# Kernel optimization log

Hardware: AMD Instinct MI355X
Metric: run time of the kernel (lower is better)

Reference implementation:

```python
import jax, jax.numpy as jnp
import numpy as np

# ---- straight-through binary quantizers (custom VJP matches torch autograd.Functions) ----
@jax.custom_vjp
def bq(x):
    return jnp.sign(x)
def _bq_fwd(x):
    return jnp.sign(x), x
def _bq_bwd(x, g):
    return (g * ((x > -1.0) & (x < 1.0)).astype(g.dtype),)
bq.defvjp(_bq_fwd, _bq_bwd)

@jax.custom_vjp
def bq_quad(x):
    return jnp.sign(x)
def _bqq_fwd(x):
    return jnp.sign(x), x
def _bqq_bwd(x, g):
    return (jnp.maximum(2.0 - jnp.abs(2.0 * x), 0.0) * g,)
bq_quad.defvjp(_bqq_fwd, _bqq_bwd)

def bilinear(x, W, s, b):
    # BiLinear: row-centered sign weights scaled by learned per-row factor, sign activations
    Wc = W - jnp.mean(W, axis=-1, keepdims=True)
    Wb = s * bq(Wc)                      # (out, in)
    return bq(x) @ Wb.T + b

def selective_scan(u, delta, A, Bs, Cs, D, delta_bias):
    # u, delta: (B,K,Dn,L); A: (K,Dn,N); Bs,Cs: (B,K,N,L); D, delta_bias: (K,Dn)
    Bn, K, Dn, L = u.shape
    N = A.shape[-1]
    delta = jax.nn.softplus(delta + delta_bias[None, :, :, None])
    def step(h, inp):
        ut, dt, Bt, Ct = inp             # (B,K,Dn),(B,K,Dn),(B,K,N),(B,K,N)
        dA = jnp.exp(dt[..., None] * A[None])
        h = dA * h + (dt * ut)[..., None] * Bt[:, :, None, :]
        y = jnp.einsum('bkdn,bkn->bkd', h, Ct)
        return h, y
    h0 = jnp.zeros((Bn, K, Dn, N), u.dtype)
    _, ys = jax.lax.scan(step, h0,
                         (u.transpose(3, 0, 1, 2), delta.transpose(3, 0, 1, 2),
                          Bs.transpose(3, 0, 1, 2), Cs.transpose(3, 0, 1, 2)))
    y = ys.transpose(1, 2, 3, 0)         # (B,K,Dn,L)
    return y + D[None, :, :, None] * u

def _forward(x, W_in, b_in, s_in, move0_b, conv_W, conv_b, rp_b0, prelu_a, rp_b1,
             Wl, bl, sl, Wd, bd, sd, dt_bias, A_logs, Ds, ln_w, ln_b, W_out, b_out, s_out):
    Bn, H, Wi, dm = x.shape
    Dn = conv_W.shape[0]
    K = 4
    N = A_logs.shape[1]
    R = Wd.shape[2]
    L = H * Wi
    xz = bilinear(x, W_in, s_in, b_in)                  # (B,H,W,2*Dn)
    xp, z = jnp.split(xz, 2, axis=-1)
    xc = xp.transpose(0, 3, 1, 2)                       # (B,Dn,H,W)
    # BConv2d: move0 bias -> sign (quad STE) -> binary conv -> RPReLU -> residual
    t = bq_quad(xc + move0_b[None, :, None, None])
    sc = jax.lax.stop_gradient(jnp.mean(jnp.abs(conv_W), axis=(1, 2, 3), keepdims=True))
    cw = jnp.clip(conv_W, -1.0, 1.0)
    Wb = jax.lax.stop_gradient(sc * jnp.sign(conv_W) - cw) + cw
    t = jax.lax.conv_general_dilated(t, Wb, (1, 1), [(1, 1), (1, 1)],
                                     dimension_numbers=('NCHW', 'OIHW', 'NCHW'))
    t = t + conv_b[None, :, None, None]
    t = t + rp_b0[None, :, None, None]
    t = jnp.where(t >= 0, t, prelu_a[None, :, None, None] * t)
    t = t + rp_b1[None, :, None, None] + xc
    xconv = jax.nn.silu(t)
    # 4-direction scan inputs
    x_flat = xconv.reshape(Bn, Dn, L)
    x_tr = xconv.transpose(0, 1, 3, 2).reshape(Bn, Dn, L)
    x_hwwh = jnp.stack([x_flat, x_tr], axis=1)
    xs = jnp.concatenate([x_hwwh, jnp.flip(x_hwwh, axis=-1)], axis=1)   # (B,K,Dn,L)
    # NOTE: torch does .view(B,L,-1) on contiguous (B,Dn,L) slices = raw reshape (not transpose)
    xin = xs.reshape(Bn, K, L, Dn)
    x_dbl = jax.vmap(bilinear, in_axes=(1, 0, 0, 0), out_axes=1)(xin, Wl, sl, bl)  # (B,K,L,R+2N)
    x_dbl = x_dbl.transpose(0, 1, 3, 2)                                 # (B,K,R+2N,L)
    dts_r, Bs, Cs = jnp.split(x_dbl, [R, R + N], axis=2)
    dts_in = dts_r.reshape(Bn, K, L, R)  # raw reshape, matches torch .view
    dts = jax.vmap(bilinear, in_axes=(1, 0, 0, 0), out_axes=1)(dts_in, Wd, sd, bd)  # (B,K,L,Dn)
    dts = dts.transpose(0, 1, 3, 2)                                     # (B,K,Dn,L)
    A = -jnp.exp(A_logs).reshape(K, Dn, N)
    out_y = selective_scan(xs, dts, A, Bs, Cs, Ds.reshape(K, Dn), dt_bias.reshape(K, Dn))
    inv_y = jnp.flip(out_y[:, 2:4], axis=-1)
    wh_y = out_y[:, 1].reshape(Bn, Dn, Wi, H).transpose(0, 1, 3, 2).reshape(Bn, Dn, L)
    invwh_y = inv_y[:, 1].reshape(Bn, Dn, Wi, H).transpose(0, 1, 3, 2).reshape(Bn, Dn, L)
    y = out_y[:, 0] + inv_y[:, 0] + wh_y + invwh_y                      # (B,Dn,L)
    y = y.transpose(0, 2, 1).reshape(Bn, H, Wi, Dn)
    mu = jnp.mean(y, axis=-1, keepdims=True)
    var = jnp.var(y, axis=-1, keepdims=True)
    y = (y - mu) / jnp.sqrt(var + 1e-5) * ln_w + ln_b                   # LayerNorm eps=1e-5
    y = y * jax.nn.silu(z)
    return bilinear(y, W_out, s_out, b_out)

def setup_inputs():
    key = jax.random.key(0)
    ks = jax.random.split(key, 12)
    B, H, Wi, dm = 4, 64, 64, 96
    Dn, N, R, K = 192, 16, 6, 4
    u = lambda k, sh, a: jax.random.uniform(k, sh, jnp.float32, -a, a)
    x = jax.random.normal(ks[0], (B, H, Wi, dm), jnp.float32)
    W_in = u(ks[1], (2 * Dn, dm), 0.015)
    b_in = u(ks[2], (2 * Dn,), 0.01)
    s_in = jnp.mean(jnp.abs(W_in), axis=1, keepdims=True)
    move0_b = jnp.zeros((Dn,), jnp.float32)
    conv_W = 0.05 * jax.random.normal(ks[3], (Dn, Dn, 3, 3), jnp.float32)
    conv_b = u(ks[4], (Dn,), 0.01)
    rp_b0 = jnp.zeros((Dn,), jnp.float32)
    prelu_a = 0.25 * jnp.ones((Dn,), jnp.float32)
    rp_b1 = jnp.zeros((Dn,), jnp.float32)
    Wl = u(ks[5], (K, R + 2 * N, Dn), 0.015)
    bl = u(ks[6], (K, R + 2 * N), 0.01)
    sl = jnp.mean(jnp.abs(Wl), axis=2, keepdims=True)
    std = R ** -0.5
    Wd = u(ks[7], (K, Dn, R), std)
    bd = u(ks[8], (K, Dn), 0.01)
    sd = jnp.mean(jnp.abs(Wd), axis=2, keepdims=True)
    dt = jnp.exp(jax.random.uniform(ks[9], (K * Dn,), jnp.float32)
                 * (np.log(0.1) - np.log(0.001)) + np.log(0.001))
    dt = jnp.clip(dt, 1e-4, None)
    dt_bias = dt + jnp.log(-jnp.expm1(-dt))
    A_logs = jnp.tile(jnp.log(jnp.arange(1, N + 1, dtype=jnp.float32))[None, :], (K * Dn, 1))
    Ds = jnp.ones((K * Dn,), jnp.float32)
    ln_w = jnp.ones((Dn,), jnp.float32)
    ln_b = jnp.zeros((Dn,), jnp.float32)
    W_out = u(ks[10], (dm, Dn), 0.015)
    b_out = u(ks[11], (dm,), 0.01)
    s_out = jnp.mean(jnp.abs(W_out), axis=1, keepdims=True)
    return dict(x=x, W_in=W_in, b_in=b_in, s_in=s_in, move0_b=move0_b, conv_W=conv_W,
                conv_b=conv_b, rp_b0=rp_b0, prelu_a=prelu_a, rp_b1=rp_b1, Wl=Wl, bl=bl,
                sl=sl, Wd=Wd, bd=bd, sd=sd, dt_bias=dt_bias, A_logs=A_logs, Ds=Ds,
                ln_w=ln_w, ln_b=ln_b, W_out=W_out, b_out=b_out, s_out=s_out)

def reference(x, W_in, b_in, s_in, move0_b, conv_W, conv_b, rp_b0, prelu_a, rp_b1,
              Wl, bl, sl, Wd, bd, sd, dt_bias, A_logs, Ds, ln_w, ln_b, W_out, b_out, s_out):
    return _forward(x, W_in, b_in, s_in, move0_b, conv_W, conv_b, rp_b0, prelu_a, rp_b1,
                    Wl, bl, sl, Wd, bd, sd, dt_bias, A_logs, Ds, ln_w, ln_b, W_out, b_out, s_out)
```

## Files before the change

### kernel.cpp

```cpp
#include <hip/hip_runtime.h>
#include <math.h>
#include <stdint.h>

#define BB 4
#define HH 64
#define WW2 64
#define DM 96
#define DN 192
#define KK 4
#define NN 16
#define RR 6
#define LL 4096
#define RN 38

#define LOG2E 1.4426950408889634f
#define LN2   0.6931471805599453f

#define OFF_WDB      0
#define OFF_WCS      4608
#define OFF_WAUX     15360
#define OFF_WSC      16896
#define OFF_WBIB     17088
#define OFF_WOUTB    18240
#define OFF_WLBB     18816
#define OFF_XBP      19728
#define OFF_PXS      19728
#define OFF_SSUM     19728
#define OFF_YB       19728
#define OFF_XC       412992
#define OFF_ZS       3558720
#define OFF_XCONV    6704448
#define OFF_XS       9850176
#define OFF_XDBL     22433088
#define OFF_HEND     OFF_XCONV

#define PLANE 4356

__device__ __forceinline__ float fsign(float v) {
  return (v > 0.f) ? 1.f : ((v < 0.f) ? -1.f : 0.f);
}
__device__ __forceinline__ float softplusf(float v) {
  return fmaxf(v, 0.f) + LN2 * log2f(1.f + exp2f(-fabsf(v) * LOG2E));
}
__device__ __forceinline__ float siluf(float v) {
  return v / (1.f + expf(-v));
}
__device__ __forceinline__ float waveAllSum(float s) {
  #pragma unroll
  for (int off = 32; off; off >>= 1) s += __shfl_xor(s, off, 64);
  return s;
}

__global__ __launch_bounds__(64) void k_prep(
    const float* __restrict__ W_in, const float* __restrict__ s_in,
    const float* __restrict__ W_out, const float* __restrict__ s_out,
    const float* __restrict__ Wl, const float* __restrict__ sl,
    const float* __restrict__ Wd, const float* __restrict__ sd,
    const float* __restrict__ convW, float* __restrict__ ws) {
  int r = blockIdx.x, lane = threadIdx.x;
  if (r < 384) {
    const float* row = W_in + r * DM;
    float s = 0.f;
    for (int c = lane; c < DM; c += 64) s += row[c];
    s = waveAllSum(s);
    float mean = s / (float)DM;
    if (lane < 3) {
      uint32_t wv = 0;
      #pragma unroll
      for (int i = 0; i < 32; ++i) wv |= (row[lane * 32 + i] - mean > 0.f ? 1u : 0u) << i;
      ((uint32_t*)(ws + OFF_WBIB))[r * 3 + lane] = wv;
    }
  } else if (r < 480) {
    int m = r - 384;
    const float* row = W_out + m * DN;
    float s = 0.f;
    for (int c = lane; c < DN; c += 64) s += row[c];
    s = waveAllSum(s);
    float mean = s / (float)DN;
    if (lane < 6) {
      uint32_t wv = 0;
      #pragma unroll
      for (int i = 0; i < 32; ++i) wv |= (row[lane * 32 + i] - mean > 0.f ? 1u : 0u) << i;
      ((uint32_t*)(ws + OFF_WOUTB))[m * 6 + lane] = wv;
    }
  } else if (r < 632) {
    int idx = r - 480;
    const float* row = Wl + idx * DN;
    float s = 0.f;
    for (int c = lane; c < DN; c += 64) s += row[c];
    s = waveAllSum(s);
    float mean = s / (float)DN;
    if (lane < 6) {
      uint32_t wv = 0;
      #pragma unroll
      for (int i = 0; i < 32; ++i) wv |= (row[lane * 32 + i] - mean > 0.f ? 1u : 0u) << i;
      ((uint32_t*)(ws + OFF_WLBB))[idx * 6 + lane] = wv;
    }
  } else if (r < 1400) {
    int idx = r - 632;
    const float* row = Wd + idx * RR;
    float s = (lane < RR) ? row[lane] : 0.f;
    s = waveAllSum(s);
    float mean = s / (float)RR;
    unsigned long long mb = __ballot((lane < RR) && (row[lane] - mean > 0.f));
    if (lane == 0) {
      ((uint32_t*)(ws + OFF_WDB))[idx] = (uint32_t)mb & 0x3Fu;
      (ws + OFF_WDB)[768 + idx] = sd[idx];
    }
  } else {
    int o = r - 1400;
    const float* row = convW + o * 1728;
    float s = 0.f;
    for (int j = lane; j < 1728; j += 64) s += fabsf(row[j]);
    s = waveAllSum(s);
    float sc = s / 1728.f;
    uint32_t* wb = (uint32_t*)(ws + OFF_WCS);
    int* aux = (int*)(ws + OFF_WAUX);
    float* scf = ws + OFF_WSC;
    uint32_t word = 0;
    if (lane < 54) {
      int cw = lane / 9, tap = lane % 9;
      #pragma unroll
      for (int i = 0; i < 32; ++i)
        word |= (row[(cw * 32 + i) * 9 + tap] > 0.f ? 1u : 0u) << i;
      wb[o * 56 + lane] = word;
    } else if (lane < 56) {
      wb[o * 56 + lane] = 0u;
    }
    int pc = (lane < 54) ? 2 * (int)__popc(word) - 32 : 0;
    int tapid = lane % 9;
    int wst = 0;
    #pragma unroll
    for (int cw = 0; cw < 6; ++cw) wst += __shfl(pc, cw * 9 + tapid, 64);
    int w_t[9];
    #pragma unroll
    for (int t9 = 0; t9 < 9; ++t9) w_t[t9] = __shfl(wst, t9, 64);
    if (lane == 0) {
      aux[o * 8 + 0] = w_t[0] + w_t[3] + w_t[6];
      aux[o * 8 + 1] = w_t[2] + w_t[5] + w_t[8];
      aux[o * 8 + 2] = w_t[0] + w_t[1] + w_t[2];
      aux[o * 8 + 3] = w_t[6] + w_t[7] + w_t[8];
      aux[o * 8 + 4] = w_t[0];
      aux[o * 8 + 5] = w_t[2];
      aux[o * 8 + 6] = w_t[6];
      aux[o * 8 + 7] = w_t[8];
      scf[o] = sc;
    }
  }
}

__global__ __launch_bounds__(384) void k_bilin_in(
    const float* __restrict__ x, const float* __restrict__ b_in,
    const float* __restrict__ s_in, const float* __restrict__ ws,
    float* __restrict__ xc, float* __restrict__ zs) {
  __shared__ uint32_t spx[16 * 3];
  __shared__ float sxz[384 * 17];
  int p0 = blockIdx.x * 16;
  if (threadIdx.x < 48) {
    int pix = threadIdx.x / 3, wd = threadIdx.x % 3;
    const float* base = x + (size_t)(p0 + pix) * DM + wd * 32;
    uint32_t wv = 0;
    #pragma unroll
    for (int i = 0; i < 32; ++i) wv |= (base[i] > 0.f ? 1u : 0u) << i;
    spx[pix * 3 + wd] = wv;
  }
  __syncthreads();
  int o = threadIdx.x;
  uint32_t w0, w1, w2;
  {
    const uint32_t* wb = (const uint32_t*)(ws + OFF_WBIB) + o * 3;
    w0 = wb[0]; w1 = wb[1]; w2 = wb[2];
  }
  float bias = b_in[o], sc = s_in[o];
  #pragma unroll
  for (int pix = 0; pix < 16; ++pix) {
    int P = (int)__popc(spx[pix * 3 + 0] ^ w0) + (int)__popc(spx[pix * 3 + 1] ^ w1) +
            (int)__popc(spx[pix * 3 + 2] ^ w2);
    sxz[o * 17 + pix] = bias + sc * (float)(DM - 2 * P);
  }
  __syncthreads();
  int b = p0 >> 12, l0 = p0 & 4095;
  for (int f = threadIdx.x; f < DN * 16; f += 384) {
    int od = f >> 4, pix = f & 15;
    xc[((size_t)(b * DN + od)) * LL + l0 + pix] = sxz[od * 17 + pix];
  }
  for (int f = threadIdx.x; f < DN * 16; f += 384) {
    int pix = f / DN, oz = f - pix * DN;
    zs[(size_t)(p0 + pix) * DN + oz] = siluf(sxz[(DN + oz) * 17 + pix]);
  }
}

__global__ __launch_bounds__(256) void k_pack(
    const float* __restrict__ xc, const float* __restrict__ move0,
    uint32_t* __restrict__ xb) {
  int t = blockIdx.x * 256 + threadIdx.x;
  int w2 = t & 31;
  int h = (t >> 5) & 63;
  int g = t >> 11;
  int cw = g % 6, b = g / 6;
  const float* xp = xc + ((size_t)(b * DN + cw * 32)) * LL + h * 64 + w2 * 2;
  uint32_t w0 = 0, w1 = 0;
  #pragma unroll
  for (int i = 0; i < 32; ++i) {
    float m = move0[cw * 32 + i];
    float2 v = *(const float2*)(xp + (size_t)i * LL);
    w0 |= (v.x + m > 0.f ? 1u : 0u) << i;
    w1 |= (v.y + m > 0.f ? 1u : 0u) << i;
  }
  uint32_t* plane = xb + (size_t)(b * 6 + cw) * PLANE;
  plane[(h + 1) * 66 + 1 + w2 * 2] = w0;
  plane[(h + 1) * 66 + 2 + w2 * 2] = w1;
}

__global__ __launch_bounds__(256) void k_conv(
    const uint32_t* __restrict__ xb, const float* __restrict__ xc,
    const uint32_t* __restrict__ wbits, const int* __restrict__ aux,
    const float* __restrict__ scf, const float* __restrict__ conv_b,
    const float* __restrict__ rp_b0, const float* __restrict__ prelu_a,
    const float* __restrict__ rp_b1, float* __restrict__ xconv) {
  int og = blockIdx.x & 3;
  int stripe = (blockIdx.x >> 2) & 15;
  int b = blockIdx.x >> 6;
  int w = threadIdx.x & 63, r = threadIdx.x >> 6;
  int h = stripe * 4 + r;

  __shared__ uint32_t swb[48 * 56];
  __shared__ int saux[48 * 8];
  __shared__ float sconst[48 * 4];
  for (int i = threadIdx.x; i < 48 * 56; i += 256) swb[i] = wbits[og * (48 * 56) + i];
  for (int i = threadIdx.x; i < 48 * 8; i += 256) saux[i] = aux[og * (48 * 8) + i];
  if (threadIdx.x < 48) {
    int o = og * 48 + threadIdx.x;
    sconst[threadIdx.x * 4 + 0] = scf[o];
    sconst[threadIdx.x * 4 + 1] = conv_b[o] + rp_b0[o];
    sconst[threadIdx.x * 4 + 2] = prelu_a[o];
    sconst[threadIdx.x * 4 + 3] = rp_b1[o];
  }

  uint32_t xw[6][9];
  const uint32_t* xpb = xb + (size_t)b * 6 * PLANE;
  #pragma unroll
  for (int cw = 0; cw < 6; ++cw) {
    const uint32_t* plane = xpb + cw * PLANE + (h + 1) * 66 + (w + 1);
    #pragma unroll
    for (int dy = 0; dy < 3; ++dy) {
      #pragma unroll
      for (int dx = 0; dx < 3; ++dx)
        xw[cw][dy * 3 + dx] = plane[(dy - 1) * 66 + (dx - 1)];
    }
  }
  bool isL = (w == 0), isR = (w == 63);
  bool isT = (h == 0), isB = (h == 63);
  const float* xcp = xc + ((size_t)(b * DN + og * 48)) * LL + h * 64 + w;
  float* xop = xconv + ((size_t)(b * DN + og * 48)) * LL + h * 64 + w;
  __syncthreads();

  #pragma unroll 1
  for (int oc = 0; oc < 48; ++oc) {
    const uint32_t* wp = &swb[oc * 56];
    int P = 0;
    #pragma unroll
    for (int cw = 0; cw < 6; ++cw) {
      int pp = 0;
      #pragma unroll
      for (int t = 0; t < 9; ++t) pp += (int)__popc(wp[cw * 9 + t] ^ xw[cw][t]);
      P += pp;
    }
    int corr = isL ? saux[oc * 8 + 0] : (isR ? saux[oc * 8 + 1] : 0);
    if (isT) {
      corr += saux[oc * 8 + 2];
      if (isL) corr -= saux[oc * 8 + 4];
      if (isR) corr -= saux[oc * 8 + 5];
    }
    if (isB) {
      corr += saux[oc * 8 + 3];
      if (isL) corr -= saux[oc * 8 + 6];
      if (isR) corr -= saux[oc * 8 + 7];
    }
    float acc = sconst[oc * 4 + 0] * (float)(1728 - 2 * P + corr);
    float t = acc + sconst[oc * 4 + 1];
    t = (t >= 0.f) ? t : sconst[oc * 4 + 2] * t;
    t += sconst[oc * 4 + 3] + *xcp;
    *xop = siluf(t);
    xcp += LL; xop += LL;
  }
}

__global__ __launch_bounds__(256) void k_build_xs(const float* __restrict__ xconv,
                                                  float* __restrict__ xs,
                                                  uint32_t* __restrict__ pxs) {
  __shared__ float tile[64][65];
  int bd = blockIdx.x;
  int b = bd / DN, d = bd % DN;
  const float* img = xconv + (size_t)bd * LL;
  for (int i = threadIdx.x; i < LL; i += 256)
    tile[i >> 6][i & 63] = img[i];
  __syncthreads();
  int lane = threadIdx.x & 63;
  #pragma unroll
  for (int k = 0; k < 4; ++k) {
    size_t base = ((size_t)((b * KK + k) * DN + d)) * LL;
    for (int j = threadIdx.x; j < LL; j += 256) {
      float v;
      if (k == 0)      v = tile[j >> 6][j & 63];
      else if (k == 1) v = tile[j & 63][j >> 6];
      else if (k == 2) { int t2 = 4095 - j; v = tile[t2 >> 6][t2 & 63]; }
      else             { int t2 = 4095 - j; v = tile[t2 & 63][t2 >> 6]; }
      xs[base + j] = v;
      unsigned long long m = __ballot(v > 0.f);
      if (lane == 0)       pxs[(base + j) >> 5] = (uint32_t)m;
      else if (lane == 32) pxs[(base + j) >> 5] = (uint32_t)(m >> 32);
    }
  }
}

__global__ __launch_bounds__(256) void k_xdbl(
    const uint32_t* __restrict__ pxs, const float* __restrict__ ws,
    const float* __restrict__ bl, const float* __restrict__ sl,
    float* __restrict__ xdbl) {
  int bk = blockIdx.x >> 4;
  int l = ((blockIdx.x & 15) << 8) + threadIdx.x;
  int k = bk & 3;
  __shared__ uint32_t swl[RN * 6];
  __shared__ float sbias[RN], ssc[RN];
  if (threadIdx.x < RN * 6) swl[threadIdx.x] = ((const uint32_t*)(ws + OFF_WLBB))[k * RN * 6 + threadIdx.x];
  if (threadIdx.x < RN) {
    sbias[threadIdx.x] = bl[k * RN + threadIdx.x];
    ssc[threadIdx.x] = sl[k * RN + threadIdx.x];
  }
  uint32_t xb[6];
  const uint32_t* pp = pxs + (size_t)bk * 24576 + (size_t)l * 6;
  #pragma unroll
  for (int j = 0; j < 6; ++j) xb[j] = pp[j];
  __syncthreads();
  float* xo = xdbl + (size_t)bk * (RN * LL) + l;
  #pragma unroll 1
  for (int o = 0; o < RN; ++o) {
    int P = 0;
    #pragma unroll
    for (int j = 0; j < 6; ++j) P += (int)__popc(xb[j] ^ swl[o * 6 + j]);
    xo[(size_t)o * LL] = sbias[o] + ssc[o] * (float)(DN - 2 * P);
  }
}

__device__ __forceinline__ void rpowers(float r, float* a) {
  float r2 = r * r, r3 = r2 * r, r4 = r2 * r2, r8 = r4 * r4;
  a[0] = r;       a[1] = r2;      a[2] = r3;      a[3] = r4;
  a[4] = r4 * r;  a[5] = r4 * r2; a[6] = r4 * r3; a[7] = r8;
  a[8] = r8 * r;  a[9] = r8 * r2; a[10] = r8 * r3; a[11] = r8 * r4;
  a[12] = r8 * a[4]; a[13] = r8 * a[5]; a[14] = r8 * a[6]; a[15] = r8 * r8;
}

__global__ __launch_bounds__(192) void k_scan_a(
    const float* __restrict__ xs, const float* __restrict__ xdbl,
    const float* __restrict__ ws, const float* __restrict__ bd,
    const float* __restrict__ dt_bias, const float* __restrict__ A_logs,
    float* __restrict__ hend, float* __restrict__ Ssum) {
  int c = blockIdx.x & 63;
  int bk = blockIdx.x >> 6;
  int k = bk & 3;
  int d = threadIdx.x;
  int t0 = c << 6;
  __shared__ uint32_t sdtm[64];
  __shared__ float4 sB4[256];
  float* sBf = (float*)sB4;
  const float* dtbase = xdbl + (size_t)bk * (RN * LL);
  if (d < 64) {
    const float2* p2 = (const float2*)(dtbase + t0 * 6 + d * 6);
    float2 a = p2[0], bb = p2[1], cc = p2[2];
    uint32_t m = (a.x > 0.f ? 1u : 0u) | (a.y > 0.f ? 2u : 0u) |
                 (bb.x > 0.f ? 4u : 0u) | (bb.y > 0.f ? 8u : 0u) |
                 (cc.x > 0.f ? 16u : 0u) | (cc.y > 0.f ? 32u : 0u);
    sdtm[d] = m;
  }
  {
    const float4* Bp = (const float4*)(xdbl + ((size_t)bk * RN + RR) * LL);
    for (int i = d; i < 256; i += 192) {
      int n = i >> 4, j = i & 15;
      float4 v = Bp[n * 1024 + (t0 >> 2) + j];
      sBf[(4 * j + 0) * 16 + n] = v.x;
      sBf[(4 * j + 1) * 16 + n] = v.y;
      sBf[(4 * j + 2) * 16 + n] = v.z;
      sBf[(4 * j + 3) * 16 + n] = v.w;
    }
  }
  uint32_t w6 = ((const uint32_t*)(ws + OFF_WDB))[k * DN + d];
  float sdv = (ws + OFF_WDB)[768 + k * DN + d];
  float biasd = bd[k * DN + d] + dt_bias[k * DN + d];
  float Araw[16];
  bool fok = true;
  {
    const float* ap = A_logs + (k * DN + d) * NN;
    #pragma unroll
    for (int n = 0; n < NN; ++n) {
      Araw[n] = -expf(ap[n]);
      fok = fok && (fabsf(Araw[n] + (float)(n + 1)) < 1e-3f);
    }
  }
  bool fastpath = (__ballot(fok) == ~0ull);
  float h[16];
  #pragma unroll
  for (int n = 0; n < NN; ++n) h[n] = 0.f;
  float S = 0.f;
  const float* up = xs + ((size_t)bk * DN + d) * LL + t0;
  __syncthreads();
  if (fastpath) {
    #pragma unroll 1
    for (int tt = 0; tt < 16; ++tt) {
      float4 u4 = *(const float4*)(up + 4 * tt);
      #pragma unroll
      for (int q = 0; q < 4; ++q) {
        int t = 4 * tt + q;
        float uv = (q == 0) ? u4.x : (q == 1) ? u4.y : (q == 2) ? u4.z : u4.w;
        int pc = (int)__popc(sdtm[t] ^ w6);
        float dv = softplusf(biasd + sdv * (float)(RR - 2 * pc));
        float rr = exp2f(-dv * LOG2E);
        S += dv;
        float du = dv * uv;
        float a[16];
        rpowers(rr, a);
        #pragma unroll
        for (int g = 0; g < 4; ++g) {
          float4 bv = sB4[t * 4 + g];
          h[4 * g + 0] = a[4 * g + 0] * h[4 * g + 0] + du * bv.x;
          h[4 * g + 1] = a[4 * g + 1] * h[4 * g + 1] + du * bv.y;
          h[4 * g + 2] = a[4 * g + 2] * h[4 * g + 2] + du * bv.z;
          h[4 * g + 3] = a[4 * g + 3] * h[4 * g + 3] + du * bv.w;
        }
      }
    }
  } else {
    float An[16];
    #pragma unroll
    for (int n = 0; n < NN; ++n) An[n] = Araw[n] * LOG2E;
    #pragma unroll 1
    for (int tt = 0; tt < 16; ++tt) {
      float4 u4 = *(const float4*)(up + 4 * tt);
      #pragma unroll
      for (int q = 0; q < 4; ++q) {
        int t = 4 * tt + q;
        float uv = (q == 0) ? u4.x : (q == 1) ? u4.y : (q == 2) ? u4.z : u4.w;
        int pc = (int)__popc(sdtm[t] ^ w6);
        float dv = softplusf(biasd + sdv * (float)(RR - 2 * pc));
        S += dv;
        float du = dv * uv;
        #pragma unroll
        for (int g = 0; g < 4; ++g) {
          float4 bv = sB4[t * 4 + g];
          float a0 = exp2f(dv * An[4 * g + 0]);
          float a1 = exp2f(dv * An[4 * g + 1]);
          float a2 = exp2f(dv * An[4 * g + 2]);
          float a3 = exp2f(dv * An[4 * g + 3]);
          h[4 * g + 0] = a0 * h[4 * g + 0] + du * bv.x;
          h[4 * g + 1] = a1 * h[4 * g + 1] + du * bv.y;
          h[4 * g + 2] = a2 * h[4 * g + 2] + du * bv.z;
          h[4 * g + 3] = a3 * h[4 * g + 3] + du * bv.w;
        }
      }
    }
  }
  float* hp = hend + (size_t)c * 49152 + (size_t)(bk * DN + d) * 16;
  #pragma unroll
  for (int n = 0; n < NN; n += 4)
    *(float4*)(hp + n) = make_float4(h[n], h[n + 1], h[n + 2], h[n + 3]);
  Ssum[c * 3072 + bk * DN + d] = S;
}

__global__ __launch_bounds__(256) void k_scan_b(
    const float* __restrict__ A_logs, const float* __restrict__ Ssum,
    float* __restrict__ hend) {
  int tid = blockIdx.x * 256 + threadIdx.x;
  int bkd = tid >> 4, n = tid & 15;
  int bk = bkd / DN, d = bkd - bk * DN;
  int k = bk & 3;
  float An2 = -expf(A_logs[(k * DN + d) * NN + n]) * LOG2E;
  float h = 0.f;
  float Sc = Ssum[bkd];
  float he = hend[tid];
  #pragma unroll 1
  for (int c = 0; c < 64; ++c) {
    float Sn = 0.f, hn = 0.f;
    if (c < 63) {
      Sn = Ssum[(c + 1) * 3072 + bkd];
      hn = hend[(size_t)(c + 1) * 49152 + tid];
    }
    hend[(size_t)c * 49152 + tid] = h;
    h = exp2f(An2 * Sc) * h + he;
    Sc = Sn; he = hn;
  }
}

__global__ __launch_bounds__(192) void k_scan_c(
    const float* __restrict__ xs, const float* __restrict__ xdbl,
    const float* __restrict__ ws, const float* __restrict__ bd,
    const float* __restrict__ dt_bias, const float* __restrict__ A_logs,
    const float* __restrict__ Ds, const float* __restrict__ h0buf,
    float* __restrict__ y) {
  int c = blockIdx.x & 63;
  int bk = blockIdx.x >> 6;
  int k = bk & 3;
  int d = threadIdx.x;
  int t0 = c << 6;
  __shared__ uint32_t sdtm[64];
  __shared__ float4 sB4[256];
  __shared__ float4 sC4[256];
  float* sBf = (float*)sB4;
  float* sCf = (float*)sC4;
  const float* dtbase = xdbl + (size_t)bk * (RN * LL);
  if (d < 64) {
    const float2* p2 = (const float2*)(dtbase + t0 * 6 + d * 6);
    float2 a = p2[0], bb = p2[1], cc = p2[2];
    uint32_t m = (a.x > 0.f ? 1u : 0u) | (a.y > 0.f ? 2u : 0u) |
                 (bb.x > 0.f ? 4u : 0u) | (bb.y > 0.f ? 8u : 0u) |
                 (cc.x > 0.f ? 16u : 0u) | (cc.y > 0.f ? 32u : 0u);
    sdtm[d] = m;
  }
  {
    const float4* Bp = (const float4*)(xdbl + ((size_t)bk * RN + RR) * LL);
    const float4* Cp = (const float4*)(xdbl + ((size_t)bk * RN + RR + NN) * LL);
    for (int i = d; i < 256; i += 192) {
      int n = i >> 4, j = i & 15;
      float4 v = Bp[n * 1024 + (t0 >> 2) + j];
      sBf[(4 * j + 0) * 16 + n] = v.x;
      sBf[(4 * j + 1) * 16 + n] = v.y;
      sBf[(4 * j + 2) * 16 + n] = v.z;
      sBf[(4 * j + 3) * 16 + n] = v.w;
      float4 w = Cp[n * 1024 + (t0 >> 2) + j];
      sCf[(4 * j + 0) * 16 + n] = w.x;
      sCf[(4 * j + 1) * 16 + n] = w.y;
      sCf[(4 * j + 2) * 16 + n] = w.z;
      sCf[(4 * j + 3) * 16 + n] = w.w;
    }
  }
  uint32_t w6 = ((const uint32_t*)(ws + OFF_WDB))[k * DN + d];
  float sdv = (ws + OFF_WDB)[768 + k * DN + d];
  float biasd = bd[k * DN + d] + dt_bias[k * DN + d];
  float Dd = Ds[k * DN + d];
  float Araw[16];
  bool fok = true;
  {
    const float* ap = A_logs + (k * DN + d) * NN;
    #pragma unroll
    for (int n = 0; n < NN; ++n) {
      Araw[n] = -expf(ap[n]);
      fok = fok && (fabsf(Araw[n] + (float)(n + 1)) < 1e-3f);
    }
  }
  bool fastpath = (__ballot(fok) == ~0ull);
  float h[16];
  {
    const float* hp = h0buf + (size_t)c * 49152 + (size_t)(bk * DN + d) * 16;
    #pragma unroll
    for (int n = 0; n < NN; n += 4) {
      float4 v = *(const float4*)(hp + n);
      h[n] = v.x; h[n + 1] = v.y; h[n + 2] = v.z; h[n + 3] = v.w;
    }
  }
  const float* up = xs + ((size_t)bk * DN + d) * LL + t0;
  float* yb = y + (size_t)(bk >> 2) * (LL * DN);
  __syncthreads();
  if (fastpath) {
    #pragma unroll 1
    for (int tt = 0; tt < 16; ++tt) {
      float4 u4 = *(const float4*)(up + 4 * tt);
      #pragma unroll
      for (int q = 0; q < 4; ++q) {
        int t = 4 * tt + q;
        float uv = (q == 0) ? u4.x : (q == 1) ? u4.y : (q == 2) ? u4.z : u4.w;
        int pc = (int)__popc(sdtm[t] ^ w6);
        float dv = softplusf(biasd + sdv * (float)(RR - 2 * pc));
        float rr = exp2f(-dv * LOG2E);
        float du = dv * uv;
        float yv = Dd * uv;
        float a[16];
        rpowers(rr, a);
        #pragma unroll
        for (int g = 0; g < 4; ++g) {
          float4 bv = sB4[t * 4 + g];
          float4 cv = sC4[t * 4 + g];
          h[4 * g + 0] = a[4 * g + 0] * h[4 * g + 0] + du * bv.x;
          h[4 * g + 1] = a[4 * g + 1] * h[4 * g + 1] + du * bv.y;
          h[4 * g + 2] = a[4 * g + 2] * h[4 * g + 2] + du * bv.z;
          h[4 * g + 3] = a[4 * g + 3] * h[4 * g + 3] + du * bv.w;
          yv += cv.x * h[4 * g + 0];
          yv += cv.y * h[4 * g + 1];
          yv += cv.z * h[4 * g + 2];
          yv += cv.w * h[4 * g + 3];
        }
        int ta = t0 + t, l;
        if (k == 0)      l = ta;
        else if (k == 1) l = ((ta & 63) << 6) | (ta >> 6);
        else if (k == 2) l = 4095 - ta;
        else { int t2 = 4095 - ta; l = ((t2 & 63) << 6) | (t2 >> 6); }
        atomicAdd(&yb[(size_t)l * DN + d], yv);
      }
    }
  } else {
    float An[16];
    #pragma unroll
    for (int n = 0; n < NN; ++n) An[n] = Araw[n] * LOG2E;
    #pragma unroll 1
    for (int tt = 0; tt < 16; ++tt) {
      float4 u4 = *(const float4*)(up + 4 * tt);
      #pragma unroll
      for (int q = 0; q < 4; ++q) {
        int t = 4 * tt + q;
        float uv = (q == 0) ? u4.x : (q == 1) ? u4.y : (q == 2) ? u4.z : u4.w;
        int pc = (int)__popc(sdtm[t] ^ w6);
        float dv = softplusf(biasd + sdv * (float)(RR - 2 * pc));
        float du = dv * uv;
        float yv = Dd * uv;
        #pragma unroll
        for (int g = 0; g < 4; ++g) {
          float4 bv = sB4[t * 4 + g];
          float4 cv = sC4[t * 4 + g];
          float a0 = exp2f(dv * An[4 * g + 0]);
          float a1 = exp2f(dv * An[4 * g + 1]);
          float a2 = exp2f(dv * An[4 * g + 2]);
          float a3 = exp2f(dv * An[4 * g + 3]);
          h[4 * g + 0] = a0 * h[4 * g + 0] + du * bv.x;
          h[4 * g + 1] = a1 * h[4 * g + 1] + du * bv.y;
          h[4 * g + 2] = a2 * h[4 * g + 2] + du * bv.z;
          h[4 * g + 3] = a3 * h[4 * g + 3] + du * bv.w;
          yv += cv.x * h[4 * g + 0];
          yv += cv.y * h[4 * g + 1];
          yv += cv.z * h[4 * g + 2];
          yv += cv.w * h[4 * g + 3];
        }
        int ta = t0 + t, l;
        if (k == 0)      l = ta;
        else if (k == 1) l = ((ta & 63) << 6) | (ta >> 6);
        else if (k == 2) l = 4095 - ta;
        else { int t2 = 4095 - ta; l = ((t2 & 63) << 6) | (t2 >> 6); }
        atomicAdd(&yb[(size_t)l * DN + d], yv);
      }
    }
  }
}

__global__ __launch_bounds__(256) void k_ln(
    const float* __restrict__ y, const float* __restrict__ zs,
    const float* __restrict__ ln_w, const float* __restrict__ ln_b,
    uint32_t* __restrict__ ybits) {
  __shared__ float ty[64 * 193];
  __shared__ float ps[256];
  __shared__ float smu[64], srs[64];
  __shared__ float slw[DN], slb[DN];
  int b = blockIdx.x >> 6;
  int l0 = (blockIdx.x & 63) << 6;
  const float* yp = y + (size_t)(b * LL + l0) * DN;
  if (threadIdx.x < DN) {
    slw[threadIdx.x] = ln_w[threadIdx.x];
    slb[threadIdx.x] = ln_b[threadIdx.x];
  }
  {
    int lc = threadIdx.x / DN, d2 = threadIdx.x - lc * DN;
    for (int i = threadIdx.x; i < 64 * DN; i += 256) {
      ty[lc * 193 + d2] = yp[i];
      d2 += 256;
      if (d2 >= DN) { d2 -= DN; lc += 1; if (d2 >= DN) { d2 -= DN; lc += 1; } }
    }
  }
  __syncthreads();
  int lc = threadIdx.x & 63, part = threadIdx.x >> 6;
  float s = 0.f;
  for (int d = part * 48; d < part * 48 + 48; ++d) s += ty[lc * 193 + d];
  ps[threadIdx.x] = s;
  __syncthreads();
  if (threadIdx.x < 64)
    smu[threadIdx.x] = (ps[threadIdx.x] + ps[threadIdx.x + 64] +
                        ps[threadIdx.x + 128] + ps[threadIdx.x + 192]) / (float)DN;
  __syncthreads();
  float mu = smu[lc];
  float q = 0.f;
  for (int d = part * 48; d < part * 48 + 48; ++d) {
    float v = ty[lc * 193 + d] - mu; q += v * v;
  }
  ps[threadIdx.x] = q;
  __syncthreads();
  if (threadIdx.x < 64) {
    float var = (ps[threadIdx.x] + ps[threadIdx.x + 64] +
                 ps[threadIdx.x + 128] + ps[threadIdx.x + 192]) / (float)DN;
    srs[threadIdx.x] = rsqrtf(var + 1e-5f);
  }
  __syncthreads();
  for (int item = threadIdx.x; item < 64 * 6; item += 256) {
    int lc2 = item / 6, wd = item % 6;
    float mu2 = smu[lc2], rs2 = srs[lc2];
    const float* zb = zs + (size_t)(b * LL + l0 + lc2) * DN + wd * 32;
    uint32_t wv = 0;
    #pragma unroll
    for (int i = 0; i < 32; ++i) {
      int d = wd * 32 + i;
      float ln = (ty[lc2 * 193 + d] - mu2) * rs2 * slw[d] + slb[d];
      wv |= ((ln * zb[i] > 0.f) ? 1u : 0u) << i;
    }
    ybits[(size_t)(b * LL + l0 + lc2) * 6 + wd] = wv;
  }
}

__global__ __launch_bounds__(256) void k_out(
    const uint32_t* __restrict__ ybits, const float* __restrict__ ws,
    const float* __restrict__ b_out, const float* __restrict__ s_out,
    float* __restrict__ out) {
  __shared__ uint32_t sy[64 * 6];
  __shared__ uint32_t swo[96 * 6];
  __shared__ float sb[96], ssc[96];
  int p0 = blockIdx.x * 64;
  for (int i = threadIdx.x; i < 64 * 6; i += 256) sy[i] = ybits[(size_t)p0 * 6 + i];
  for (int i = threadIdx.x; i < 96 * 6; i += 256) swo[i] = ((const uint32_t*)(ws + OFF_WOUTB))[i];
  if (threadIdx.x < 96) {
    sb[threadIdx.x] = b_out[threadIdx.x];
    ssc[threadIdx.x] = s_out[threadIdx.x];
  }
  __syncthreads();
  for (int oi = threadIdx.x; oi < 64 * DM; oi += 256) {
    int pr = oi / DM, m = oi % DM;
    int P = 0;
    #pragma unroll
    for (int j = 0; j < 6; ++j) P += (int)__popc(sy[pr * 6 + j] ^ swo[m * 6 + j]);
    out[(size_t)(p0 + pr) * DM + m] = sb[m] + ssc[m] * (float)(DN - 2 * P);
  }
}

extern "C" void kernel_launch(void* const* d_in, const int* in_sizes, int n_in,
                              void* d_out, int out_size, void* d_ws, size_t ws_size,
                              hipStream_t stream) {
  const float* x       = (const float*)d_in[0];
  const float* W_in    = (const float*)d_in[1];
  const float* b_in    = (const float*)d_in[2];
  const float* s_in    = (const float*)d_in[3];
  const float* move0_b = (const float*)d_in[4];
  const float* conv_W  = (const float*)d_in[5];
  const float* conv_b  = (const float*)d_in[6];
  const float* rp_b0   = (const float*)d_in[7];
  const float* prelu_a = (const float*)d_in[8];
  const float* rp_b1   = (const float*)d_in[9];
  const float* Wl      = (const float*)d_in[10];
  const float* bl      = (const float*)d_in[11];
  const float* sl      = (const float*)d_in[12];
  const float* Wd      = (const float*)d_in[13];
  const float* bd      = (const float*)d_in[14];
  const float* sd      = (const float*)d_in[15];
  const float* dt_bias = (const float*)d_in[16];
  const float* A_logs  = (const float*)d_in[17];
  const float* Ds      = (const float*)d_in[18];
  const float* ln_w    = (const float*)d_in[19];
  const float* ln_b    = (const float*)d_in[20];
  const float* W_out   = (const float*)d_in[21];
  const float* b_out   = (const float*)d_in[22];
  const float* s_out   = (const float*)d_in[23];
  float* ws  = (float*)d_ws;
  float* out = (float*)d_out;

  hipLaunchKernelGGL(k_prep, dim3(1592), dim3(64), 0, stream,
                     W_in, s_in, W_out, s_out, Wl, sl, Wd, sd, conv_W, ws);
  hipLaunchKernelGGL(k_bilin_in, dim3(1024), dim3(384), 0, stream,
                     x, b_in, s_in, ws, ws + OFF_XC, ws + OFF_ZS);
  hipMemsetAsync((void*)(ws + OFF_XBP), 0, (size_t)(4 * 6 * PLANE) * 4, stream);
  hipLaunchKernelGGL(k_pack, dim3(192), dim3(256), 0, stream,
                     ws + OFF_XC, move0_b, (uint32_t*)(ws + OFF_XBP));
  hipLaunchKernelGGL(k_conv, dim3(256), dim3(256), 0, stream,
                     (const uint32_t*)(ws + OFF_XBP), ws + OFF_XC,
                     (const uint32_t*)(ws + OFF_WCS), (const int*)(ws + OFF_WAUX),
                     ws + OFF_WSC, conv_b, rp_b0, prelu_a, rp_b1,
                     ws + OFF_XCONV);
  hipLaunchKernelGGL(k_build_xs, dim3(768), dim3(256), 0, stream,
                     ws + OFF_XCONV, ws + OFF_XS, (uint32_t*)(ws + OFF_PXS));
  hipLaunchKernelGGL(k_xdbl, dim3(256), dim3(256), 0, stream,
                     (const uint32_t*)(ws + OFF_PXS), ws, bl, sl, ws + OFF_XDBL);
  hipLaunchKernelGGL(k_scan_a, dim3(1024), dim3(192), 0, stream,
                     ws + OFF_XS, ws + OFF_XDBL, ws, bd, dt_bias, A_logs,
                     ws + OFF_HEND, ws + OFF_SSUM);
  hipLaunchKernelGGL(k_scan_b, dim3(192), dim3(256), 0, stream,
                     A_logs, ws + OFF_SSUM, ws + OFF_HEND);
  hipMemsetAsync((void*)(ws + OFF_XC), 0, (size_t)3145728 * sizeof(float), stream);
  hipLaunchKernelGGL(k_scan_c, dim3(1024), dim3(192), 0, stream,
                     ws + OFF_XS, ws + OFF_XDBL, ws, bd, dt_bias, A_logs, Ds,
                     ws + OFF_HEND, ws + OFF_XC);
  hipLaunchKernelGGL(k_ln, dim3(256), dim3(256), 0, stream,
                     ws + OFF_XC, ws + OFF_ZS, ln_w, ln_b, (uint32_t*)(ws + OFF_YB));
  hipLaunchKernelGGL(k_out, dim3(256), dim3(256), 0, stream,
                     (const uint32_t*)(ws + OFF_YB), ws, b_out, s_out, out);
}
```

Before: 341.8 us.

## Split scan state across two thread halves, tabulate softplus, fuse sign-pack into bilinear

The scan kernels now use 384 threads per block, with each half holding 8 of the 16 state channels. Because the dt projection has only 7 possible popcount outcomes, softplus and its decay values are precomputed per channel into shared-memory tables. The decay powers are built from a base (r or r^9) times a short multiplication ladder. The separate sign-pack kernel is folded into the input bilinear kernel, and k_prep stages conv weights in shared memory before bit-packing. These changes double the parallelism of the latency-bound recurrence, cut transcendental math from the inner loop and remove one launch and one read of xc, at the cost of more shared memory and redundant B/dt loads per block.

```diff
diff --git a/kernel.cpp b/kernel.cpp
--- a/kernel.cpp
+++ b/kernel.cpp
@@ -57,6 +57,7 @@
     const float* __restrict__ Wl, const float* __restrict__ sl,
     const float* __restrict__ Wd, const float* __restrict__ sd,
     const float* __restrict__ convW, float* __restrict__ ws) {
+  __shared__ float srow[1728];
   int r = blockIdx.x, lane = threadIdx.x;
   if (r < 384) {
     const float* row = W_in + r * DM;
@@ -111,8 +112,13 @@
     int o = r - 1400;
     const float* row = convW + o * 1728;
     float s = 0.f;
-    for (int j = lane; j < 1728; j += 64) s += fabsf(row[j]);
+    for (int j = lane; j < 1728; j += 64) {
+      float v = row[j];
+      srow[j] = v;
+      s += fabsf(v);
+    }
     s = waveAllSum(s);
+    __syncthreads();
     float sc = s / 1728.f;
     uint32_t* wb = (uint32_t*)(ws + OFF_WCS);
     int* aux = (int*)(ws + OFF_WAUX);
@@ -122,7 +128,7 @@
       int cw = lane / 9, tap = lane % 9;
       #pragma unroll
       for (int i = 0; i < 32; ++i)
-        word |= (row[(cw * 32 + i) * 9 + tap] > 0.f ? 1u : 0u) << i;
+        word |= (srow[(cw * 32 + i) * 9 + tap] > 0.f ? 1u : 0u) << i;
       wb[o * 56 + lane] = word;
     } else if (lane < 56) {
       wb[o * 56 + lane] = 0u;
@@ -151,10 +157,12 @@
 
 __global__ __launch_bounds__(384) void k_bilin_in(
     const float* __restrict__ x, const float* __restrict__ b_in,
-    const float* __restrict__ s_in, const float* __restrict__ ws,
-    float* __restrict__ xc, float* __restrict__ zs) {
+    const float* __restrict__ s_in, const float* __restrict__ move0,
+    const float* __restrict__ ws, float* __restrict__ xc, float* __restrict__ zs,
+    uint32_t* __restrict__ xb) {
   __shared__ uint32_t spx[16 * 3];
   __shared__ float sxz[384 * 17];
+  __shared__ float smv[DN];
   int p0 = blockIdx.x * 16;
   if (threadIdx.x < 48) {
     int pix = threadIdx.x / 3, wd = threadIdx.x % 3;
@@ -164,6 +172,7 @@
     for (int i = 0; i < 32; ++i) wv |= (base[i] > 0.f ? 1u : 0u) << i;
     spx[pix * 3 + wd] = wv;
   }
+  if (threadIdx.x < DN) smv[threadIdx.x] = move0[threadIdx.x];
   __syncthreads();
   int o = threadIdx.x;
   uint32_t w0, w1, w2;
@@ -188,28 +197,18 @@
     int pix = f / DN, oz = f - pix * DN;
     zs[(size_t)(p0 + pix) * DN + oz] = siluf(sxz[(DN + oz) * 17 + pix]);
   }
-}
-
-__global__ __launch_bounds__(256) void k_pack(
-    const float* __restrict__ xc, const float* __restrict__ move0,
-    uint32_t* __restrict__ xb) {
-  int t = blockIdx.x * 256 + threadIdx.x;
-  int w2 = t & 31;
-  int h = (t >> 5) & 63;
-  int g = t >> 11;
-  int cw = g % 6, b = g / 6;
-  const float* xp = xc + ((size_t)(b * DN + cw * 32)) * LL + h * 64 + w2 * 2;
-  uint32_t w0 = 0, w1 = 0;
-  #pragma unroll
-  for (int i = 0; i < 32; ++i) {
-    float m = move0[cw * 32 + i];
-    float2 v = *(const float2*)(xp + (size_t)i * LL);
-    w0 |= (v.x + m > 0.f ? 1u : 0u) << i;
-    w1 |= (v.y + m > 0.f ? 1u : 0u) << i;
-  }
-  uint32_t* plane = xb + (size_t)(b * 6 + cw) * PLANE;
-  plane[(h + 1) * 66 + 1 + w2 * 2] = w0;
-  plane[(h + 1) * 66 + 2 + w2 * 2] = w1;
+  if (threadIdx.x < 96) {
+    int pix = threadIdx.x / 6, cw = threadIdx.x % 6;
+    uint32_t wv = 0;
+    #pragma unroll
+    for (int i = 0; i < 32; ++i) {
+      int dch = cw * 32 + i;
+      wv |= ((sxz[dch * 17 + pix] + smv[dch] > 0.f) ? 1u : 0u) << i;
+    }
+    int l = l0 + pix, h = l >> 6, w = l & 63;
+    uint32_t* plane = xb + (size_t)(b * 6 + cw) * PLANE;
+    plane[(h + 1) * 66 + 1 + w] = wv;
+  }
 }
 
 __global__ __launch_bounds__(256) void k_conv(
@@ -343,15 +342,19 @@
   }
 }
 
-__device__ __forceinline__ void rpowers(float r, float* a) {
-  float r2 = r * r, r3 = r2 * r, r4 = r2 * r2, r8 = r4 * r4;
-  a[0] = r;       a[1] = r2;      a[2] = r3;      a[3] = r4;
-  a[4] = r4 * r;  a[5] = r4 * r2; a[6] = r4 * r3; a[7] = r8;
-  a[8] = r8 * r;  a[9] = r8 * r2; a[10] = r8 * r3; a[11] = r8 * r4;
-  a[12] = r8 * a[4]; a[13] = r8 * a[5]; a[14] = r8 * a[6]; a[15] = r8 * r8;
-}
-
-__global__ __launch_bounds__(192) void k_scan_a(
+__device__ __forceinline__ void ladder8(float base, float r, float* a) {
+  float r2 = r * r, r4 = r2 * r2;
+  a[0] = base;
+  a[1] = base * r;
+  a[2] = base * r2;
+  a[3] = a[1] * r2;
+  a[4] = base * r4;
+  a[5] = a[1] * r4;
+  a[6] = a[2] * r4;
+  a[7] = a[3] * r4;
+}
+
+__global__ __launch_bounds__(384) void k_scan_a(
     const float* __restrict__ xs, const float* __restrict__ xdbl,
     const float* __restrict__ ws, const float* __restrict__ bd,
     const float* __restrict__ dt_bias, const float* __restrict__ A_logs,
@@ -359,23 +362,26 @@
   int c = blockIdx.x & 63;
   int bk = blockIdx.x >> 6;
   int k = bk & 3;
-  int d = threadIdx.x;
+  int tid = threadIdx.x;
+  int half = (tid >= 192) ? 1 : 0;
+  int d = tid - half * 192;
   int t0 = c << 6;
   __shared__ uint32_t sdtm[64];
   __shared__ float4 sB4[256];
+  __shared__ float sDV[192 * 9], sR[192 * 9], sR9[192 * 9];
   float* sBf = (float*)sB4;
   const float* dtbase = xdbl + (size_t)bk * (RN * LL);
-  if (d < 64) {
-    const float2* p2 = (const float2*)(dtbase + t0 * 6 + d * 6);
+  if (tid < 64) {
+    const float2* p2 = (const float2*)(dtbase + t0 * 6 + tid * 6);
     float2 a = p2[0], bb = p2[1], cc = p2[2];
     uint32_t m = (a.x > 0.f ? 1u : 0u) | (a.y > 0.f ? 2u : 0u) |
                  (bb.x > 0.f ? 4u : 0u) | (bb.y > 0.f ? 8u : 0u) |
                  (cc.x > 0.f ? 16u : 0u) | (cc.y > 0.f ? 32u : 0u);
-    sdtm[d] = m;
+    sdtm[tid] = m;
   }
   {
     const float4* Bp = (const float4*)(xdbl + ((size_t)bk * RN + RR) * LL);
-    for (int i = d; i < 256; i += 192) {
+    for (int i = tid; i < 256; i += 384) {
       int n = i >> 4, j = i & 15;
       float4 v = Bp[n * 1024 + (t0 >> 2) + j];
       sBf[(4 * j + 0) * 16 + n] = v.x;
@@ -387,20 +393,34 @@
   uint32_t w6 = ((const uint32_t*)(ws + OFF_WDB))[k * DN + d];
   float sdv = (ws + OFF_WDB)[768 + k * DN + d];
   float biasd = bd[k * DN + d] + dt_bias[k * DN + d];
-  float Araw[16];
+  if (!half) {
+    #pragma unroll
+    for (int pc = 0; pc < 7; ++pc) {
+      float dv = softplusf(biasd + sdv * (float)(RR - 2 * pc));
+      sDV[d * 9 + pc] = dv;
+      sR[d * 9 + pc] = exp2f(-dv * LOG2E);
+    }
+  } else {
+    #pragma unroll
+    for (int pc = 0; pc < 7; ++pc) {
+      float dv = softplusf(biasd + sdv * (float)(RR - 2 * pc));
+      sR9[d * 9 + pc] = exp2f(-9.f * dv * LOG2E);
+    }
+  }
+  float Araw[8];
   bool fok = true;
   {
-    const float* ap = A_logs + (k * DN + d) * NN;
-    #pragma unroll
-    for (int n = 0; n < NN; ++n) {
+    const float* ap = A_logs + (k * DN + d) * NN + half * 8;
+    #pragma unroll
+    for (int n = 0; n < 8; ++n) {
       Araw[n] = -expf(ap[n]);
-      fok = fok && (fabsf(Araw[n] + (float)(n + 1)) < 1e-3f);
+      fok = fok && (fabsf(Araw[n] + (float)(n + 1 + half * 8)) < 1e-3f);
     }
   }
   bool fastpath = (__ballot(fok) == ~0ull);
-  float h[16];
+  float h[8];
   #pragma unroll
-  for (int n = 0; n < NN; ++n) h[n] = 0.f;
+  for (int n = 0; n < 8; ++n) h[n] = 0.f;
   float S = 0.f;
   const float* up = xs + ((size_t)bk * DN + d) * LL + t0;
   __syncthreads();
@@ -413,15 +433,16 @@
         int t = 4 * tt + q;
         float uv = (q == 0) ? u4.x : (q == 1) ? u4.y : (q == 2) ? u4.z : u4.w;
         int pc = (int)__popc(sdtm[t] ^ w6);
-        float dv = softplusf(biasd + sdv * (float)(RR - 2 * pc));
-        float rr = exp2f(-dv * LOG2E);
+        float dv = sDV[d * 9 + pc];
+        float r = sR[d * 9 + pc];
+        float base = half ? sR9[d * 9 + pc] : r;
         S += dv;
         float du = dv * uv;
-        float a[16];
-        rpowers(rr, a);
+        float a[8];
+        ladder8(base, r, a);
         #pragma unroll
-        for (int g = 0; g < 4; ++g) {
-          float4 bv = sB4[t * 4 + g];
+        for (int g = 0; g < 2; ++g) {
+          float4 bv = sB4[t * 4 + half * 2 + g];
           h[4 * g + 0] = a[4 * g + 0] * h[4 * g + 0] + du * bv.x;
           h[4 * g + 1] = a[4 * g + 1] * h[4 * g + 1] + du * bv.y;
           h[4 * g + 2] = a[4 * g + 2] * h[4 * g + 2] + du * bv.z;
@@ -430,9 +451,9 @@
       }
     }
   } else {
-    float An[16];
-    #pragma unroll
-    for (int n = 0; n < NN; ++n) An[n] = Araw[n] * LOG2E;
+    float An[8];
+    #pragma unroll
+    for (int n = 0; n < 8; ++n) An[n] = Araw[n] * LOG2E;
     #pragma unroll 1
     for (int tt = 0; tt < 16; ++tt) {
       float4 u4 = *(const float4*)(up + 4 * tt);
@@ -441,12 +462,12 @@
         int t = 4 * tt + q;
         float uv = (q == 0) ? u4.x : (q == 1) ? u4.y : (q == 2) ? u4.z : u4.w;
         int pc = (int)__popc(sdtm[t] ^ w6);
-        float dv = softplusf(biasd + sdv * (float)(RR - 2 * pc));
+        float dv = sDV[d * 9 + pc];
         S += dv;
         float du = dv * uv;
         #pragma unroll
-        for (int g = 0; g < 4; ++g) {
-          float4 bv = sB4[t * 4 + g];
+        for (int g = 0; g < 2; ++g) {
+          float4 bv = sB4[t * 4 + half * 2 + g];
           float a0 = exp2f(dv * An[4 * g + 0]);
           float a1 = exp2f(dv * An[4 * g + 1]);
           float a2 = exp2f(dv * An[4 * g + 2]);
@@ -459,11 +480,10 @@
       }
     }
   }
-  float* hp = hend + (size_t)c * 49152 + (size_t)(bk * DN + d) * 16;
-  #pragma unroll
-  for (int n = 0; n < NN; n += 4)
-    *(float4*)(hp + n) = make_float4(h[n], h[n + 1], h[n + 2], h[n + 3]);
-  Ssum[c * 3072 + bk * DN + d] = S;
+  float* hp = hend + (size_t)c * 49152 + (size_t)(bk * DN + d) * 16 + half * 8;
+  *(float4*)(hp + 0) = make_float4(h[0], h[1], h[2], h[3]);
+  *(float4*)(hp + 4) = make_float4(h[4], h[5], h[6], h[7]);
+  if (!half) Ssum[c * 3072 + bk * DN + d] = S;
 }
 
 __global__ __launch_bounds__(256) void k_scan_b(
@@ -490,7 +510,7 @@
   }
 }
 
-__global__ __launch_bounds__(192) void k_scan_c(
+__global__ __launch_bounds__(384) void k_scan_c(
     const float* __restrict__ xs, const float* __restrict__ xdbl,
     const float* __restrict__ ws, const float* __restrict__ bd,
     const float* __restrict__ dt_bias, const float* __restrict__ A_logs,
@@ -499,26 +519,29 @@
   int c = blockIdx.x & 63;
   int bk = blockIdx.x >> 6;
   int k = bk & 3;
-  int d = threadIdx.x;
+  int tid = threadIdx.x;
+  int half = (tid >= 192) ? 1 : 0;
+  int d = tid - half * 192;
   int t0 = c << 6;
   __shared__ uint32_t sdtm[64];
   __shared__ float4 sB4[256];
   __shared__ float4 sC4[256];
+  __shared__ float sDV[192 * 9], sR[192 * 9], sR9[192 * 9];
   float* sBf = (float*)sB4;
   float* sCf = (float*)sC4;
   const float* dtbase = xdbl + (size_t)bk * (RN * LL);
-  if (d < 64) {
-    const float2* p2 = (const float2*)(dtbase + t0 * 6 + d * 6);
+  if (tid < 64) {
+    const float2* p2 = (const float2*)(dtbase + t0 * 6 + tid * 6);
     float2 a = p2[0], bb = p2[1], cc = p2[2];
     uint32_t m = (a.x > 0.f ? 1u : 0u) | (a.y > 0.f ? 2u : 0u) |
                  (bb.x > 0.f ? 4u : 0u) | (bb.y > 0.f ? 8u : 0u) |
                  (cc.x > 0.f ? 16u : 0u) | (cc.y > 0.f ? 32u : 0u);
-    sdtm[d] = m;
+    sdtm[tid] = m;
   }
   {
     const float4* Bp = (const float4*)(xdbl + ((size_t)bk * RN + RR) * LL);
     const float4* Cp = (const float4*)(xdbl + ((size_t)bk * RN + RR + NN) * LL);
-    for (int i = d; i < 256; i += 192) {
+    for (int i = tid; i < 256; i += 384) {
       int n = i >> 4, j = i & 15;
       float4 v = Bp[n * 1024 + (t0 >> 2) + j];
       sBf[(4 * j + 0) * 16 + n] = v.x;
@@ -536,28 +559,42 @@
   float sdv = (ws + OFF_WDB)[768 + k * DN + d];
   float biasd = bd[k * DN + d] + dt_bias[k * DN + d];
   float Dd = Ds[k * DN + d];
-  float Araw[16];
+  if (!half) {
+    #pragma unroll
+    for (int pc = 0; pc < 7; ++pc) {
+      float dv = softplusf(biasd + sdv * (float)(RR - 2 * pc));
+      sDV[d * 9 + pc] = dv;
+      sR[d * 9 + pc] = exp2f(-dv * LOG2E);
+    }
+  } else {
+    #pragma unroll
+    for (int pc = 0; pc < 7; ++pc) {
+      float dv = softplusf(biasd + sdv * (float)(RR - 2 * pc));
+      sR9[d * 9 + pc] = exp2f(-9.f * dv * LOG2E);
+    }
+  }
+  float Araw[8];
   bool fok = true;
   {
-    const float* ap = A_logs + (k * DN + d) * NN;
-    #pragma unroll
-    for (int n = 0; n < NN; ++n) {
+    const float* ap = A_logs + (k * DN + d) * NN + half * 8;
+    #pragma unroll
+    for (int n = 0; n < 8; ++n) {
       Araw[n] = -expf(ap[n]);
-      fok = fok && (fabsf(Araw[n] + (float)(n + 1)) < 1e-3f);
+      fok = fok && (fabsf(Araw[n] + (float)(n + 1 + half * 8)) < 1e-3f);
     }
   }
   bool fastpath = (__ballot(fok) == ~0ull);
-  float h[16];
+  float h[8];
   {
-    const float* hp = h0buf + (size_t)c * 49152 + (size_t)(bk * DN + d) * 16;
-    #pragma unroll
-    for (int n = 0; n < NN; n += 4) {
-      float4 v = *(const float4*)(hp + n);
-      h[n] = v.x; h[n + 1] = v.y; h[n + 2] = v.z; h[n + 3] = v.w;
-    }
+    const float* hp = h0buf + (size_t)c * 49152 + (size_t)(bk * DN + d) * 16 + half * 8;
+    float4 v0 = *(const float4*)(hp + 0);
+    float4 v1 = *(const float4*)(hp + 4);
+    h[0] = v0.x; h[1] = v0.y; h[2] = v0.z; h[3] = v0.w;
+    h[4] = v1.x; h[5] = v1.y; h[6] = v1.z; h[7] = v1.w;
   }
   const float* up = xs + ((size_t)bk * DN + d) * LL + t0;
   float* yb = y + (size_t)(bk >> 2) * (LL * DN);
+  float Dh = half ? 0.f : Dd;
   __syncthreads();
   if (fastpath) {
     #pragma unroll 1
@@ -568,16 +605,17 @@
         int t = 4 * tt + q;
         float uv = (q == 0) ? u4.x : (q == 1) ? u4.y : (q == 2) ? u4.z : u4.w;
         int pc = (int)__popc(sdtm[t] ^ w6);
-        float dv = softplusf(biasd + sdv * (float)(RR - 2 * pc));
-        float rr = exp2f(-dv * LOG2E);
+        float dv = sDV[d * 9 + pc];
+        float r = sR[d * 9 + pc];
+        float base = half ? sR9[d * 9 + pc] : r;
         float du = dv * uv;
-        float yv = Dd * uv;
-        float a[16];
-        rpowers(rr, a);
+        float yv = Dh * uv;
+        float a[8];
+        ladder8(base, r, a);
         #pragma unroll
-        for (int g = 0; g < 4; ++g) {
-          float4 bv = sB4[t * 4 + g];
-          float4 cv = sC4[t * 4 + g];
+        for (int g = 0; g < 2; ++g) {
+          float4 bv = sB4[t * 4 + half * 2 + g];
+          float4 cv = sC4[t * 4 + half * 2 + g];
           h[4 * g + 0] = a[4 * g + 0] * h[4 * g + 0] + du * bv.x;
           h[4 * g + 1] = a[4 * g + 1] * h[4 * g + 1] + du * bv.y;
           h[4 * g + 2] = a[4 * g + 2] * h[4 * g + 2] + du * bv.z;
@@ -596,9 +634,9 @@
       }
     }
   } else {
-    float An[16];
-    #pragma unroll
-    for (int n = 0; n < NN; ++n) An[n] = Araw[n] * LOG2E;
+    float An[8];
+    #pragma unroll
+    for (int n = 0; n < 8; ++n) An[n] = Araw[n] * LOG2E;
     #pragma unroll 1
     for (int tt = 0; tt < 16; ++tt) {
       float4 u4 = *(const float4*)(up + 4 * tt);
@@ -607,13 +645,13 @@
         int t = 4 * tt + q;
         float uv = (q == 0) ? u4.x : (q == 1) ? u4.y : (q == 2) ? u4.z : u4.w;
         int pc = (int)__popc(sdtm[t] ^ w6);
-        float dv = softplusf(biasd + sdv * (float)(RR - 2 * pc));
+        float dv = sDV[d * 9 + pc];
         float du = dv * uv;
-        float yv = Dd * uv;
+        float yv = Dh * uv;
         #pragma unroll
-        for (int g = 0; g < 4; ++g) {
-          float4 bv = sB4[t * 4 + g];
-          float4 cv = sC4[t * 4 + g];
+        for (int g = 0; g < 2; ++g) {
+          float4 bv = sB4[t * 4 + half * 2 + g];
+          float4 cv = sC4[t * 4 + half * 2 + g];
           float a0 = exp2f(dv * An[4 * g + 0]);
           float a1 = exp2f(dv * An[4 * g + 1]);
           float a2 = exp2f(dv * An[4 * g + 2]);
@@ -755,11 +793,10 @@
 
   hipLaunchKernelGGL(k_prep, dim3(1592), dim3(64), 0, stream,
                      W_in, s_in, W_out, s_out, Wl, sl, Wd, sd, conv_W, ws);
+  hipMemsetAsync((void*)(ws + OFF_XBP), 0, (size_t)(4 * 6 * PLANE) * 4, stream);
   hipLaunchKernelGGL(k_bilin_in, dim3(1024), dim3(384), 0, stream,
-                     x, b_in, s_in, ws, ws + OFF_XC, ws + OFF_ZS);
-  hipMemsetAsync((void*)(ws + OFF_XBP), 0, (size_t)(4 * 6 * PLANE) * 4, stream);
-  hipLaunchKernelGGL(k_pack, dim3(192), dim3(256), 0, stream,
-                     ws + OFF_XC, move0_b, (uint32_t*)(ws + OFF_XBP));
+                     x, b_in, s_in, move0_b, ws, ws + OFF_XC, ws + OFF_ZS,
+                     (uint32_t*)(ws + OFF_XBP));
   hipLaunchKernelGGL(k_conv, dim3(256), dim3(256), 0, stream,
                      (const uint32_t*)(ws + OFF_XBP), ws + OFF_XC,
                      (const uint32_t*)(ws + OFF_WCS), (const int*)(ws + OFF_WAUX),
@@ -769,13 +806,13 @@
                      ws + OFF_XCONV, ws + OFF_XS, (uint32_t*)(ws + OFF_PXS));
   hipLaunchKernelGGL(k_xdbl, dim3(256), dim3(256), 0, stream,
                      (const uint32_t*)(ws + OFF_PXS), ws, bl, sl, ws + OFF_XDBL);
-  hipLaunchKernelGGL(k_scan_a, dim3(1024), dim3(192), 0, stream,
+  hipLaunchKernelGGL(k_scan_a, dim3(1024), dim3(384), 0, stream,
                      ws + OFF_XS, ws + OFF_XDBL, ws, bd, dt_bias, A_logs,
                      ws + OFF_HEND, ws + OFF_SSUM);
   hipLaunchKernelGGL(k_scan_b, dim3(192), dim3(256), 0, stream,
                      A_logs, ws + OFF_SSUM, ws + OFF_HEND);
   hipMemsetAsync((void*)(ws + OFF_XC), 0, (size_t)3145728 * sizeof(float), stream);
-  hipLaunchKernelGGL(k_scan_c, dim3(1024), dim3(192), 0, stream,
+  hipLaunchKernelGGL(k_scan_c, dim3(1024), dim3(384), 0, stream,
                      ws + OFF_XS, ws + OFF_XDBL, ws, bd, dt_bias, A_logs, Ds,
                      ws + OFF_HEND, ws + OFF_XC);
   hipLaunchKernelGGL(k_ln, dim3(256), dim3(256), 0, stream,
```

Result: slower. 363.5 us (+6.3%).
